# Kernel tuning notes

Measured on AMD Instinct MI355X. Metric: run time of the kernel, lower is better.

The kernel has to match this reference:

```python
import jax, jax.numpy as jnp
import numpy as np

B, L, D, V, M = 8, 64, 256, 4096, 16


def _norm(a):
    # torch .std(-1) uses ddof=1 (unbiased)
    return a / (1e-5 + jnp.std(a, axis=-1, keepdims=True, ddof=1))


def setup_inputs() -> dict:
    key = jax.random.key(0)
    ks = jax.random.split(key, 13)
    s = 0.05
    return {
        "x": jax.random.randint(ks[0], (B, L), 0, V),
        "z": jax.random.randint(ks[1], (B, L), 0, V),
        "embed_w": jax.random.normal(ks[2], (V, D), dtype=jnp.float32) * s,
        "init_w": jax.random.normal(ks[3], (D, M), dtype=jnp.float32) * s,
        "trans_w": jax.random.normal(ks[4], (D, D), dtype=jnp.float32) * s,
        "trans_b": jax.random.normal(ks[5], (D,), dtype=jnp.float32) * s,
        "core_w": jax.random.normal(ks[6], (D, D), dtype=jnp.float32) * s,
        "upd_w": jax.random.normal(ks[7], (D, D), dtype=jnp.float32) * s,
        "xks_w": jax.random.normal(ks[8], (2, D), dtype=jnp.float32) * s,
        "xkd_w": jax.random.normal(ks[9], (D, D), dtype=jnp.float32) * s,
        "xkd_b": jax.random.normal(ks[10], (D,), dtype=jnp.float32) * s,
        "emi_w": jax.random.normal(ks[11], (D, D), dtype=jnp.float32) * s,
        "emi_b": jax.random.normal(ks[12], (D,), dtype=jnp.float32) * s,
    }


def reference(x, z, embed_w, init_w, trans_w, trans_b, core_w, upd_w,
              xks_w, xkd_w, xkd_b, emi_w, emi_b):
    # loss() sets y = x * 0 (all-zero token ids)
    ze = _norm(embed_w[z])                      # (B, L, D)
    ye = _norm(embed_w[x * 0])                  # (B, L, D)
    Bq, Lq, Dq = ze.shape

    # init_state.weight.T[None, 0:1] -> column 0, broadcast to (B, L, D), then norm
    xsa0 = _norm(jnp.broadcast_to(init_w[:, 0][None, None, :], (Bq, Lq, Dq)))

    def step(xsa, _):
        xnew = (jnp.roll(xsa, 1, axis=1) @ trans_w
                + jnp.roll(xsa, -1, axis=1) @ trans_w.T
                + xsa @ core_w
                + ze @ upd_w.T
                + trans_b) / 3.0
        return xnew, None

    xsa, _ = jax.lax.scan(step, xsa0, None, length=Lq)

    # mixture head
    xkey_static = jnp.broadcast_to(xks_w[None], (Bq, 2, Dq))          # (B, 2, D)
    xkey_dynamic = ye @ xkd_w.T + xkd_b                                # (B, L, D)
    xkey = jnp.concatenate([xkey_static, xkey_dynamic], axis=1)       # (B, 2+L, D)

    emit = xsa @ emi_w.T + emi_b                                       # (B, L, D)
    cand = jnp.concatenate(
        [emit[:, :, None], ze[:, :, None],
         jnp.broadcast_to(ye[:, None], (Bq, Lq, Lq, Dq))], axis=2)     # (B, L, 2+L, D)

    sel = jax.nn.log_softmax(jnp.einsum('bld,bkd->blk', xsa, xkey), axis=-1)  # (B, L, 2+L)
    lptok_c = jax.nn.log_softmax(cand @ embed_w.T, axis=-1)            # (B, L, 2+L, V)
    lptok = jax.nn.logsumexp(sel[..., None] + lptok_c, axis=-2)        # (B, L, V)
    lptok = jnp.exp(lptok / 2.0)

    cent = jnp.take_along_axis(lptok, x[:, :, None], axis=-1)[..., 0]  # (B, L)
    return -cent.mean(-1)                                              # (B,)
```

## Files before the change

### kernel.cpp

```cpp
#include <hip/hip_runtime.h>
#include <hip/hip_bf16.h>
#include <math.h>

#define BB 8
#define LL 64
#define DD 256
#define VV 4096
#define RR 512
#define K3 768

typedef __attribute__((ext_vector_type(4))) float f32x4;
typedef __attribute__((ext_vector_type(8))) short bf16x8;
typedef __attribute__((ext_vector_type(4))) unsigned short u16x4;
typedef unsigned long long u64;

#define WS_ZE      0
#define WS_ZEU3    (WS_ZE + RR*DD)
#define WS_WCT     (WS_ZEU3 + RR*DD)
#define WS_XSA0    (WS_WCT + DD*K3)
#define WS_XSA1    (WS_XSA0 + RR*DD)
#define WS_EMIT    (WS_XSA1 + RR*DD)
#define WS_YVEC    (WS_EMIT + RR*DD)
#define WS_X0VEC   (WS_YVEC + DD)
#define WS_YK      (WS_X0VEC + DD)
#define WS_YLOG    (WS_YK + DD)
#define WS_YLSE    (WS_YLOG + VV)
#define WS_SEL     (WS_YLSE + 8)
#define WS_TOKS    WS_SEL
#define WS_HPART   WS_WCT
#define WS_TWT     WS_XSA0
#define WS_CWT     (WS_XSA0 + 65536)
#define WS_EHI     861184
#define WS_ELO     (WS_EHI + VV*DD/2)

__device__ __forceinline__ float waveSum(float v) {
#pragma unroll
  for (int o = 32; o > 0; o >>= 1) v += __shfl_xor(v, o, 64);
  return v;
}

__device__ __forceinline__ unsigned short f2bf(float f) {
  unsigned int u = __float_as_uint(f);
  unsigned int r = (u + 0x7fffu + ((u >> 16) & 1u)) >> 16;
  return (unsigned short)r;
}
__device__ __forceinline__ float bf2f(unsigned short h) {
  return __uint_as_float(((unsigned int)h) << 16);
}

union U64F2 { u64 u; float f[2]; };

__global__ __launch_bounds__(256) void k_prep1(
    const int* __restrict__ z, const float* __restrict__ embed,
    const float* __restrict__ initw, const float* __restrict__ tw,
    const float* __restrict__ cw, float* __restrict__ ws) {
  int bid = blockIdx.x, d = threadIdx.x;
  __shared__ float red[4];
  if (bid < RR + 2) {
    float a; float* dst;
    if (bid < RR) { int tok = z[bid]; a = embed[tok * DD + d]; dst = ws + WS_ZE + bid * DD; }
    else if (bid == RR) { a = embed[d]; dst = ws + WS_YVEC; }
    else { a = initw[d * 16]; dst = ws + WS_X0VEC; }
    int lane = d & 63, w = d >> 6;
    float s = waveSum(a);
    __syncthreads();
    if (lane == 0) red[w] = s;
    __syncthreads();
    float sum = red[0] + red[1] + red[2] + red[3];
    float sq = waveSum(a * a);
    __syncthreads();
    if (lane == 0) red[w] = sq;
    __syncthreads();
    float sqs = red[0] + red[1] + red[2] + red[3];
    float mean = sum * (1.0f / DD);
    float var = fmaxf((sqs - (float)DD * mean * mean) * (1.0f / (DD - 1)), 0.0f);
    dst[d] = a / (1e-5f + sqrtf(var));
  } else {
    int c = bid - (RR + 2);
    ws[WS_TWT + c * DD + d] = tw[d * DD + c];
    ws[WS_CWT + c * DD + d] = cw[d * DD + c];
  }
}

__global__ __launch_bounds__(256) void k_rowmat2(
    const float* __restrict__ in, const float* __restrict__ W,
    const float* __restrict__ bias, float* __restrict__ out, float scale) {
  int r0 = blockIdx.x * 2, d = threadIdx.x;
  __shared__ float u[2][260];
  u[0][d] = in[r0 * DD + d];
  u[1][d] = in[(r0 + 1) * DD + d];
  __syncthreads();
  float a0 = 0.f, a1 = 0.f;
  const float4* w4 = (const float4*)(W + d * DD);
  const float4* u0 = (const float4*)&u[0][0];
  const float4* u1 = (const float4*)&u[1][0];
#pragma unroll 8
  for (int k4 = 0; k4 < 64; k4++) {
    float4 w = w4[k4], x0 = u0[k4], x1 = u1[k4];
    a0 += x0.x*w.x + x0.y*w.y + x0.z*w.z + x0.w*w.w;
    a1 += x1.x*w.x + x1.y*w.y + x1.z*w.z + x1.w*w.w;
  }
  float b = bias[d];
  out[r0 * DD + d]       = (a0 + b) * scale;
  out[(r0 + 1) * DD + d] = (a1 + b) * scale;
}

__global__ __launch_bounds__(256) void k_prep3(
    const float* __restrict__ tw, const float* __restrict__ cw,
    float* __restrict__ ws) {
  int bid = blockIdx.x, c = threadIdx.x;
  __shared__ float zs[4][260];
  __shared__ float rA[DD], rB[DD], rC[DD];
  if (bid < 256) {
    int r0 = bid * 2;
    int b = r0 >> 6, l = r0 & 63;
    const float* zb = ws + WS_ZEU3 + (size_t)b * 64 * DD;
    float* zout = ws + WS_XSA1;
#pragma unroll
    for (int j = 0; j < 4; ++j) {
      int ll = (l + j - 1 + 64) & 63;
      zs[j][c] = zb[ll * DD + c];
    }
    __syncthreads();
    const float4* wA = (const float4*)(ws + WS_TWT + (size_t)c * DD);
    const float4* wB = (const float4*)(tw + (size_t)c * DD);
    const float4* wC = (const float4*)(ws + WS_CWT + (size_t)c * DD);
    const float4* zm0 = (const float4*)&zs[0][0];
    const float4* z00 = (const float4*)&zs[1][0];
    const float4* zp0 = (const float4*)&zs[2][0];
    const float4* zp1 = (const float4*)&zs[3][0];
    float a0 = 0.f, a1 = 0.f;
#pragma unroll 8
    for (int k4 = 0; k4 < 64; ++k4) {
      float4 A4 = wA[k4], B4 = wB[k4], C4 = wC[k4];
      float4 m0 = zm0[k4], z0 = z00[k4], p0 = zp0[k4], p1 = zp1[k4];
      a0 += m0.x*A4.x + m0.y*A4.y + m0.z*A4.z + m0.w*A4.w
          + p0.x*B4.x + p0.y*B4.y + p0.z*B4.z + p0.w*B4.w
          + z0.x*C4.x + z0.y*C4.y + z0.z*C4.z + z0.w*C4.w;
      a1 += z0.x*A4.x + z0.y*A4.y + z0.z*A4.z + z0.w*A4.w
          + p1.x*B4.x + p1.y*B4.y + p1.z*B4.z + p1.w*B4.w
          + p0.x*C4.x + p0.y*C4.y + p0.z*C4.z + p0.w*C4.w;
    }
    const float inv3 = 1.0f / 3.0f;
    zout[(size_t)r0 * DD + c]       = a0 * inv3 + zs[1][c];
    zout[(size_t)(r0 + 1) * DD + c] = a1 * inv3 + zs[2][c];
  } else if (bid < 512) {
    int k = bid - 256;
    const float* twT = ws + WS_TWT;
    const float inv9 = 1.0f / 9.0f;
    rA[c] = tw[k * DD + c] * inv9;
    rB[c] = twT[k * DD + c] * inv9;
    rC[c] = cw[k * DD + c] * inv9;
    __syncthreads();
    float a2 = 0.f, m1 = 0.f, m0 = 0.f, m3 = 0.f, b2 = 0.f;
#pragma unroll 4
    for (int j = 0; j < DD; ++j) {
      float Aj = tw[j * DD + c];
      float Bj = twT[j * DD + c];
      float Cj = cw[j * DD + c];
      float ra = rA[j], rb = rB[j], rc = rC[j];
      a2 += ra * Aj;
      m1 += rc * Aj + ra * Cj;
      m0 += rb * Aj + ra * Bj + rc * Cj;
      m3 += rc * Bj + rb * Cj;
      b2 += rb * Bj;
    }
    float* p0 = ws + WS_WCT;
    float* p3 = ws + WS_ZEU3;
    p0[k * DD + c]               = a2;
    p0[65536 + k * DD + c]       = m1;
    p0[2 * 65536 + k * DD + c]   = m0;
    p3[k * DD + c]               = m3;
    p3[65536 + k * DD + c]       = b2;
  } else {
    ((int*)(ws + WS_TOKS))[(bid - 512) * 256 + c] = 0;
  }
}

__global__ __launch_bounds__(256, 2) void k_scan_big(
    float* __restrict__ ws, const float* __restrict__ embed,
    const float* __restrict__ emiw, const float* __restrict__ emib) {
  const int bid = blockIdx.x;
  const int t = threadIdx.x, lane = t & 63;

  __shared__ float S[12 * 264];
  __shared__ float PAR[32 * 260];
  __shared__ float PAR2[4 * 256];
  __shared__ float ZB[256];

  if (bid >= 512) {
    int eb = bid - 512;
    if (eb < 1024) {
      unsigned short* eh = (unsigned short*)(ws + WS_EHI);
      unsigned short* el = (unsigned short*)(ws + WS_ELO);
      int i = (eb * 256 + t) * 4;
      float4 v = *(const float4*)(embed + i);
      float f[4] = {v.x, v.y, v.z, v.w};
      u16x4 h, l;
#pragma unroll
      for (int j = 0; j < 4; ++j) {
        unsigned short hb = f2bf(f[j]);
        h[j] = hb;
        l[j] = f2bf(f[j] - bf2f(hb));
      }
      *(u16x4*)(eh + i) = h;
      *(u16x4*)(el + i) = l;
    } else {
      int yb = eb - 1024;
      float* y = S;
      y[t] = ws[WS_YVEC + t];
      __syncthreads();
      int w = t >> 6;
      for (int i = 0; i < 16; i++) {
        int v = yb * 64 + i * 4 + w;
        float p = 0.f;
#pragma unroll
        for (int j = 0; j < 4; j++)
          p += y[lane + 64*j] * embed[(size_t)v * DD + lane + 64*j];
        p = waveSum(p);
        if (lane == 0) ws[WS_YLOG + v] = p;
      }
    }
    return;
  }

  const int rg = bid & 63, cg = bid >> 6;
  const int b = rg >> 3, rgl = rg & 7, l0 = rgl * 8;
  const int cl = t & 7, rs = t >> 3;
  const int c0 = cg * 32 + cl * 4;

  int* tok = (int*)(ws + WS_TOKS);

  const float* Wp[5] = {ws + WS_WCT, ws + WS_WCT + 65536, ws + WS_WCT + 2*65536,
                        ws + WS_ZEU3, ws + WS_ZEU3 + 65536};
  f32x4 wreg[40];
#pragma unroll
  for (int p = 0; p < 5; ++p)
#pragma unroll
    for (int q = 0; q < 2; ++q)
#pragma unroll
      for (int kk = 0; kk < 4; ++kk)
        wreg[p * 8 + q * 4 + kk] =
            *(const f32x4*)&Wp[p][(size_t)(rs * 8 + q * 4 + kk) * DD + c0];

  {
    int r = t >> 5, c = t & 31;
    ZB[r * 32 + c] = ws[WS_XSA1 + (size_t)(b * 64 + l0 + r) * DD + cg * 32 + c];
  }

  const int nb0 = b * 8 + ((rgl + 7) & 7);
  const int nb1 = b * 8 + rgl;
  const int nb2 = b * 8 + ((rgl + 1) & 7);
  const int myl = (lane == 0) ? nb0 : (lane == 1) ? nb1 : nb2;

  for (int st = 0; st < 32; ++st) {
    const float* xin  = ws + ((st & 1) ? WS_XSA1 : WS_XSA0);
    float*       xout = ws + ((st & 1) ? WS_XSA0 : WS_XSA1);

    if (st > 0) {
      const int tg = st << 3;
      while (true) {
        int v = __hip_atomic_load(tok + myl * 32, __ATOMIC_RELAXED,
                                  __HIP_MEMORY_SCOPE_AGENT);
        if (__all(v >= tg)) break;
        __builtin_amdgcn_s_sleep(1);
      }
    }

#pragma unroll
    for (int it = 0; it < 6; ++it) {
      int idx = it * 256 + t;
      int j = idx >> 7;
      int kk = (idx & 127) << 1;
      const u64* src = (st == 0)
          ? (const u64*)(ws + WS_X0VEC + kk)
          : (const u64*)(xin + (size_t)(b * 64 + ((l0 + j - 2 + 64) & 63)) * DD + kk);
      u64 v = __hip_atomic_load(src, __ATOMIC_RELAXED, __HIP_MEMORY_SCOPE_AGENT);
      *(u64*)(&S[j * 264 + kk]) = v;
    }
    __syncthreads();

    f32x4 acc[8];
#pragma unroll
    for (int r = 0; r < 8; ++r) acc[r] = (f32x4){0.f, 0.f, 0.f, 0.f};

#pragma unroll
    for (int p = 0; p < 5; ++p) {
#pragma unroll
      for (int r = 0; r < 8; ++r) {
        int j = r + p;
#pragma unroll
        for (int q = 0; q < 2; ++q) {
          f32x4 xv = *(const f32x4*)&S[j * 264 + rs * 8 + q * 4];
          acc[r] += xv.x * wreg[p * 8 + q * 4 + 0];
          acc[r] += xv.y * wreg[p * 8 + q * 4 + 1];
          acc[r] += xv.z * wreg[p * 8 + q * 4 + 2];
          acc[r] += xv.w * wreg[p * 8 + q * 4 + 3];
        }
      }
    }

#pragma unroll
    for (int r = 0; r < 8; ++r)
      *(f32x4*)&PAR[rs * 260 + r * 32 + cl * 4] = acc[r];
    __syncthreads();

    {
      int u = t & 63, v = t >> 6;
      f32x4 s4 = (f32x4){0.f, 0.f, 0.f, 0.f};
#pragma unroll
      for (int i = 0; i < 8; ++i)
        s4 += *(const f32x4*)&PAR[(v * 8 + i) * 260 + u * 4];
      *(f32x4*)&PAR2[v * 256 + u * 4] = s4;
    }
    __syncthreads();

    if (t < 64) {
      int r = t >> 3, c8 = t & 7;
      f32x4 s4 = (f32x4){0.f, 0.f, 0.f, 0.f};
#pragma unroll
      for (int v = 0; v < 4; ++v)
        s4 += *(const f32x4*)&PAR2[v * 256 + t * 4];
      f32x4 zb = *(const f32x4*)&ZB[r * 32 + c8 * 4];
      s4 += zb;
      size_t off = (size_t)(b * 64 + l0 + r) * DD + cg * 32 + c8 * 4;
      U64F2 lo, hi;
      lo.f[0] = s4.x; lo.f[1] = s4.y;
      hi.f[0] = s4.z; hi.f[1] = s4.w;
      __hip_atomic_store((u64*)(xout + off),     lo.u, __ATOMIC_RELAXED, __HIP_MEMORY_SCOPE_AGENT);
      __hip_atomic_store((u64*)(xout + off + 2), hi.u, __ATOMIC_RELAXED, __HIP_MEMORY_SCOPE_AGENT);
    }

    __syncthreads();
    if (t == 0)
      __hip_atomic_fetch_add(tok + nb1 * 32, 1, __ATOMIC_RELAXED,
                             __HIP_MEMORY_SCOPE_AGENT);
  }

  if (t == 0) {
    while (__hip_atomic_load(tok + nb1 * 32, __ATOMIC_RELAXED,
                             __HIP_MEMORY_SCOPE_AGENT) < 256)
      __builtin_amdgcn_s_sleep(1);
  }
  __syncthreads();
#pragma unroll
  for (int it = 0; it < 4; ++it) {
    int idx = it * 256 + t;
    int j = idx >> 7;
    int kk = (idx & 127) << 1;
    u64 v = __hip_atomic_load(
        (const u64*)(ws + WS_XSA0 + (size_t)(b * 64 + l0 + j) * DD + kk),
        __ATOMIC_RELAXED, __HIP_MEMORY_SCOPE_AGENT);
    *(u64*)(&S[j * 264 + kk]) = v;
  }
  __syncthreads();
  {
    int r = t >> 5, c = cg * 32 + (t & 31);
    const float4* wv = (const float4*)(emiw + (size_t)c * DD);
    const float4* xv = (const float4*)&S[r * 264];
    float a = 0.f;
#pragma unroll 8
    for (int k4 = 0; k4 < 64; ++k4) {
      float4 w = wv[k4], x = xv[k4];
      a += x.x*w.x + x.y*w.y + x.z*w.z + x.w*w.w;
    }
    ws[WS_EMIT + (size_t)(b * 64 + l0 + r) * DD + c] = a + emib[c];
  }
}

__global__ __launch_bounds__(256) void k_head_mfma(
    const float* __restrict__ uemit, const float* __restrict__ uze,
    const unsigned short* __restrict__ eh, const unsigned short* __restrict__ el,
    float* __restrict__ hpart) {
  int row0 = blockIdx.x * 32;
  int v0 = blockIdx.y * 128;
  int t = threadIdx.x, lane = t & 63, w = t >> 6;
  int wr = w >> 1, wc = w & 1;
  __shared__ unsigned short UH[32 * 264];
  __shared__ unsigned short UL[32 * 264];
  const float* src = (row0 < RR) ? (uemit + (size_t)row0 * DD)
                                 : (uze + (size_t)(row0 - RR) * DD);
#pragma unroll
  for (int it = 0; it < 4; ++it) {
    int r = it * 8 + (t >> 5);
    int c8 = (t & 31) * 8;
    float4 a = *(const float4*)(src + (size_t)r * DD + c8);
    float4 b2 = *(const float4*)(src + (size_t)r * DD + c8 + 4);
    float fa[8] = {a.x, a.y, a.z, a.w, b2.x, b2.y, b2.z, b2.w};
    u16x4 h0, l0v, h1, l1;
#pragma unroll
    for (int j = 0; j < 4; ++j) {
      unsigned short hb = f2bf(fa[j]);
      h0[j] = hb; l0v[j] = f2bf(fa[j] - bf2f(hb));
      unsigned short hb1 = f2bf(fa[4 + j]);
      h1[j] = hb1; l1[j] = f2bf(fa[4 + j] - bf2f(hb1));
    }
    *(u16x4*)(&UH[r * 264 + c8])     = h0;
    *(u16x4*)(&UH[r * 264 + c8 + 4]) = h1;
    *(u16x4*)(&UL[r * 264 + c8])     = l0v;
    *(u16x4*)(&UL[r * 264 + c8 + 4]) = l1;
  }
  __syncthreads();

  f32x4 acc[4];
#pragma unroll
  for (int q = 0; q < 4; ++q) acc[q] = (f32x4){0.f, 0.f, 0.f, 0.f};

  int arow = wr * 16 + (lane & 15);
  int kof = 8 * (lane >> 4);
  const unsigned short* Ah = &UH[arow * 264 + kof];
  const unsigned short* Al = &UL[arow * 264 + kof];
  int vbase = v0 + wc * 64 + (lane & 15);

#pragma unroll
  for (int p = 0; p < 3; ++p) {
    const unsigned short* Ab = (p == 2) ? Al : Ah;
    const unsigned short* Ebl = ((p == 1) ? el : eh) + (size_t)vbase * DD + kof;
#pragma unroll
    for (int ks = 0; ks < 8; ++ks) {
      int k0 = ks * 32;
      bf16x8 a = *(const bf16x8*)(Ab + k0);
#pragma unroll
      for (int vt = 0; vt < 4; ++vt) {
        bf16x8 bfr = *(const bf16x8*)(Ebl + vt * 16 * DD + k0);
        acc[vt] = __builtin_amdgcn_mfma_f32_16x16x32_bf16(a, bfr, acc[vt], 0, 0, 0);
      }
    }
  }

  int chunk = blockIdx.y * 2 + wc;
#pragma unroll
  for (int i = 0; i < 4; ++i) {
    float mm = -1e30f;
#pragma unroll
    for (int vt = 0; vt < 4; ++vt) mm = fmaxf(mm, acc[vt][i]);
#pragma unroll
    for (int o = 1; o < 16; o <<= 1) mm = fmaxf(mm, __shfl_xor(mm, o, 64));
    float ss = 0.f;
#pragma unroll
    for (int vt = 0; vt < 4; ++vt) ss += __expf(acc[vt][i] - mm);
#pragma unroll
    for (int o = 1; o < 16; o <<= 1) ss += __shfl_xor(ss, o, 64);
    if ((lane & 15) == 0) {
      int row = row0 + wr * 16 + (lane >> 4) * 4 + i;
      hpart[(row * 64 + chunk) * 2]     = mm;
      hpart[(row * 64 + chunk) * 2 + 1] = ss;
    }
  }
}

__global__ __launch_bounds__(256) void k_finish(
    const int* __restrict__ x, const float* __restrict__ embed,
    const float* __restrict__ xks, const float* __restrict__ xkdw,
    const float* __restrict__ xkdb, float* __restrict__ ws,
    float* __restrict__ out) {
  int b = blockIdx.x, t = threadIdx.x, lane = t & 63, w = t >> 6;
  __shared__ float YK[DD];
  __shared__ float rm[4], rv[4];
  __shared__ float ylse_s;
  __shared__ float sel0[64], sel1[64], sel2[64], tg0[64], tg1[64];
  __shared__ float ls0s[64], ls1s[64];

  {
    float acc = xkdb[t];
    const float4* yv4 = (const float4*)(ws + WS_YVEC);
    const float4* w4 = (const float4*)(xkdw + (size_t)t * DD);
    float a = 0.f;
#pragma unroll 8
    for (int k4 = 0; k4 < 64; ++k4) {
      float4 yv = yv4[k4], wv = w4[k4];
      a += yv.x*wv.x + yv.y*wv.y + yv.z*wv.z + yv.w*wv.w;
    }
    YK[t] = acc + a;
  }
  {
    float m = -1e30f, s = 0.f;
    for (int v = t; v < VV; v += 256) {
      float lg = ws[WS_YLOG + v];
      float mn = fmaxf(m, lg);
      s = s * __expf(m - mn) + __expf(lg - mn);
      m = mn;
    }
#pragma unroll
    for (int o = 32; o > 0; o >>= 1) {
      float mo = __shfl_xor(m, o, 64), so = __shfl_xor(s, o, 64);
      float mn = fmaxf(m, mo);
      s = s * __expf(m - mn) + so * __expf(mo - mn);
      m = mn;
    }
    if (lane == 0) { rm[w] = m; rv[w] = s; }
  }
  __syncthreads();
  if (t == 0) {
    float M = fmaxf(fmaxf(rm[0], rm[1]), fmaxf(rm[2], rm[3]));
    float S = rv[0]*__expf(rm[0]-M) + rv[1]*__expf(rm[1]-M) +
              rv[2]*__expf(rm[2]-M) + rv[3]*__expf(rm[3]-M);
    ylse_s = M + logf(S);
  }

  const float* hp = ws + WS_HPART;
  for (int i = 0; i < 16; ++i) {
    int l = w * 16 + i, r = b * 64 + l;
    float4 xs = *(const float4*)&ws[WS_XSA0 + (size_t)r * DD + lane * 4];
    float4 k0 = *(const float4*)&xks[lane * 4];
    float4 k1 = *(const float4*)&xks[DD + lane * 4];
    float4 yk4 = *(const float4*)&YK[lane * 4];
    float s0 = waveSum(xs.x*k0.x + xs.y*k0.y + xs.z*k0.z + xs.w*k0.w);
    float s1 = waveSum(xs.x*k1.x + xs.y*k1.y + xs.z*k1.z + xs.w*k1.w);
    float s2 = waveSum(xs.x*yk4.x + xs.y*yk4.y + xs.z*yk4.z + xs.w*yk4.w);
    int xv = x[r];
    float4 e4 = *(const float4*)&embed[(size_t)xv * DD + lane * 4];
    float4 em = *(const float4*)&ws[WS_EMIT + (size_t)r * DD + lane * 4];
    float4 zr = *(const float4*)&ws[WS_ZE + (size_t)r * DD + lane * 4];
    float t0 = waveSum(em.x*e4.x + em.y*e4.y + em.z*e4.z + em.w*e4.w);
    float t1 = waveSum(zr.x*e4.x + zr.y*e4.y + zr.z*e4.z + zr.w*e4.w);
    float m0 = hp[((size_t)r * 64 + lane) * 2];
    float q0 = hp[((size_t)r * 64 + lane) * 2 + 1];
    float m1 = hp[((size_t)(RR + r) * 64 + lane) * 2];
    float q1 = hp[((size_t)(RR + r) * 64 + lane) * 2 + 1];
#pragma unroll
    for (int o = 32; o > 0; o >>= 1) {
      float mo = __shfl_xor(m0, o, 64), so = __shfl_xor(q0, o, 64);
      float mn = fmaxf(m0, mo);
      q0 = q0 * __expf(m0 - mn) + so * __expf(mo - mn);
      m0 = mn;
      mo = __shfl_xor(m1, o, 64); so = __shfl_xor(q1, o, 64);
      mn = fmaxf(m1, mo);
      q1 = q1 * __expf(m1 - mn) + so * __expf(mo - mn);
      m1 = mn;
    }
    if (lane == 0) {
      sel0[l] = s0; sel1[l] = s1; sel2[l] = s2;
      tg0[l] = t0; tg1[l] = t1;
      ls0s[l] = m0 + logf(q0);
      ls1s[l] = m1 + logf(q1);
    }
  }
  __syncthreads();
  if (w == 0) {
    int l = lane, r = b * 64 + l;
    float s0 = sel0[l], s1 = sel1[l], s2 = sel2[l];
    float mx = fmaxf(s0, fmaxf(s1, s2));
    float den = expf(s0 - mx) + expf(s1 - mx) + 64.f * expf(s2 - mx);
    float lsel = mx + logf(den);
    int xv = x[r];
    float P0 = expf(s0 - lsel + tg0[l] - ls0s[l]);
    float P1 = expf(s1 - lsel + tg1[l] - ls1s[l]);
    float Py = expf(s2 - lsel + ws[WS_YLOG + xv] - ylse_s);
    float cent = sqrtf(P0 + P1 + 64.f * Py);
    float sum = waveSum(cent);
    if (lane == 0) out[b] = -(sum * (1.0f / 64.f));
  }
}

extern "C" void kernel_launch(void* const* d_in, const int* in_sizes, int n_in,
                              void* d_out, int out_size, void* d_ws, size_t ws_size,
                              hipStream_t stream) {
  (void)in_sizes; (void)n_in; (void)out_size; (void)ws_size;
  const int*   x     = (const int*)d_in[0];
  const int*   z     = (const int*)d_in[1];
  const float* embed = (const float*)d_in[2];
  const float* initw = (const float*)d_in[3];
  const float* tw    = (const float*)d_in[4];
  const float* tb    = (const float*)d_in[5];
  const float* cw    = (const float*)d_in[6];
  const float* uw    = (const float*)d_in[7];
  const float* xks   = (const float*)d_in[8];
  const float* xkdw  = (const float*)d_in[9];
  const float* xkdb  = (const float*)d_in[10];
  const float* emiw  = (const float*)d_in[11];
  const float* emib  = (const float*)d_in[12];
  float* ws  = (float*)d_ws;
  float* out = (float*)d_out;

  hipLaunchKernelGGL(k_prep1, dim3(RR + 2 + 256), dim3(256), 0, stream,
                     z, embed, initw, tw, cw, ws);
  hipLaunchKernelGGL(k_rowmat2, dim3(256), dim3(256), 0, stream,
                     ws + WS_ZE, uw, tb, ws + WS_ZEU3, 1.0f / 3.0f);
  hipLaunchKernelGGL(k_prep3, dim3(520), dim3(256), 0, stream, tw, cw, ws);
  hipLaunchKernelGGL(k_scan_big, dim3(1600), dim3(256), 0, stream,
                     ws, embed, emiw, emib);
  hipLaunchKernelGGL(k_head_mfma, dim3(32, 32), dim3(256), 0, stream,
                     ws + WS_EMIT, ws + WS_ZE,
                     (const unsigned short*)(ws + WS_EHI),
                     (const unsigned short*)(ws + WS_ELO),
                     ws + WS_HPART);
  hipLaunchKernelGGL(k_finish, dim3(8), dim3(256), 0, stream,
                     x, embed, xks, xkdw, xkdb, ws, out);
}
```

Measured before the change: 353.4 us.

## Overlap ze-row head tiles with the scan and move embed prep earlier

Moves the bf16 hi/lo split of the embedding and the y-logit computation out of the scan kernel into the prep kernel, with a new tiny kernel that normalizes the y and x0 vectors first. When the workspace is large enough, the half of the head GEMM that depends only on ze rows runs as extra blocks inside the scan kernel, with partial results written to a separate buffer, so it overlaps the latency-bound scan. The separate head kernel then covers only the emit rows. This adds a launch, relies on workspace size to choose the path, and could cost scan occupancy through the shared memory union.

```diff
diff --git a/kernel.cpp b/kernel.cpp
--- a/kernel.cpp
+++ b/kernel.cpp
@@ -27,11 +27,12 @@
 #define WS_YLSE    (WS_YLOG + VV)
 #define WS_SEL     (WS_YLSE + 8)
 #define WS_TOKS    WS_SEL
-#define WS_HPART   WS_WCT
 #define WS_TWT     WS_XSA0
 #define WS_CWT     (WS_XSA0 + 65536)
 #define WS_EHI     861184
 #define WS_ELO     (WS_EHI + VV*DD/2)
+#define WS_HPHI    (WS_ELO + VV*DD/2)
+#define WS_BIG_FLOATS (WS_HPHI + 1024*64*2)
 
 __device__ __forceinline__ float waveSum(float v) {
 #pragma unroll
@@ -49,6 +50,86 @@
 }
 
 union U64F2 { u64 u; float f[2]; };
+
+__device__ __forceinline__ void head_tile(
+    int row0, int vy, const float* __restrict__ uemit,
+    const float* __restrict__ uze,
+    const unsigned short* __restrict__ eh, const unsigned short* __restrict__ el,
+    float* __restrict__ hpart, float* shbuf, int t) {
+  unsigned short* UH = (unsigned short*)shbuf;
+  unsigned short* UL = UH + 32 * 264;
+  int lane = t & 63, w = t >> 6;
+  int wr = w >> 1, wc = w & 1;
+  const float* src = (row0 < RR) ? (uemit + (size_t)row0 * DD)
+                                 : (uze + (size_t)(row0 - RR) * DD);
+#pragma unroll
+  for (int it = 0; it < 4; ++it) {
+    int r = it * 8 + (t >> 5);
+    int c8 = (t & 31) * 8;
+    float4 a = *(const float4*)(src + (size_t)r * DD + c8);
+    float4 b2 = *(const float4*)(src + (size_t)r * DD + c8 + 4);
+    float fa[8] = {a.x, a.y, a.z, a.w, b2.x, b2.y, b2.z, b2.w};
+    u16x4 h0, l0v, h1, l1;
+#pragma unroll
+    for (int j = 0; j < 4; ++j) {
+      unsigned short hb = f2bf(fa[j]);
+      h0[j] = hb; l0v[j] = f2bf(fa[j] - bf2f(hb));
+      unsigned short hb1 = f2bf(fa[4 + j]);
+      h1[j] = hb1; l1[j] = f2bf(fa[4 + j] - bf2f(hb1));
+    }
+    *(u16x4*)(&UH[r * 264 + c8])     = h0;
+    *(u16x4*)(&UH[r * 264 + c8 + 4]) = h1;
+    *(u16x4*)(&UL[r * 264 + c8])     = l0v;
+    *(u16x4*)(&UL[r * 264 + c8 + 4]) = l1;
+  }
+  __syncthreads();
+
+  f32x4 acc[4];
+#pragma unroll
+  for (int q = 0; q < 4; ++q) acc[q] = (f32x4){0.f, 0.f, 0.f, 0.f};
+
+  int arow = wr * 16 + (lane & 15);
+  int kof = 8 * (lane >> 4);
+  const unsigned short* Ah = &UH[arow * 264 + kof];
+  const unsigned short* Al = &UL[arow * 264 + kof];
+  int vbase = vy * 128 + wc * 64 + (lane & 15);
+
+#pragma unroll
+  for (int p = 0; p < 3; ++p) {
+    const unsigned short* Ab = (p == 2) ? Al : Ah;
+    const unsigned short* Ebl = ((p == 1) ? el : eh) + (size_t)vbase * DD + kof;
+#pragma unroll
+    for (int ks = 0; ks < 8; ++ks) {
+      int k0 = ks * 32;
+      bf16x8 a = *(const bf16x8*)(Ab + k0);
+#pragma unroll
+      for (int vt = 0; vt < 4; ++vt) {
+        bf16x8 bfr = *(const bf16x8*)(Ebl + vt * 16 * DD + k0);
+        acc[vt] = __builtin_amdgcn_mfma_f32_16x16x32_bf16(a, bfr, acc[vt], 0, 0, 0);
+      }
+    }
+  }
+
+  int chunk = vy * 2 + wc;
+#pragma unroll
+  for (int i = 0; i < 4; ++i) {
+    float mm = -1e30f;
+#pragma unroll
+    for (int vt = 0; vt < 4; ++vt) mm = fmaxf(mm, acc[vt][i]);
+#pragma unroll
+    for (int o = 1; o < 16; o <<= 1) mm = fmaxf(mm, __shfl_xor(mm, o, 64));
+    float ss = 0.f;
+#pragma unroll
+    for (int vt = 0; vt < 4; ++vt) ss += __expf(acc[vt][i] - mm);
+#pragma unroll
+    for (int o = 1; o < 16; o <<= 1) ss += __shfl_xor(ss, o, 64);
+    if ((lane & 15) == 0) {
+      int row = row0 + wr * 16 + (lane >> 4) * 4 + i;
+      hpart[((size_t)row * 64 + chunk) * 2]     = mm;
+      hpart[((size_t)row * 64 + chunk) * 2 + 1] = ss;
+    }
+  }
+}
 
 __global__ __launch_bounds__(256) void k_prep1(
     const int* __restrict__ z, const float* __restrict__ embed,
@@ -56,6 +137,7 @@
     const float* __restrict__ cw, float* __restrict__ ws) {
   int bid = blockIdx.x, d = threadIdx.x;
   __shared__ float red[4];
+  __shared__ float y[DD];
   if (bid < RR + 2) {
     float a; float* dst;
     if (bid < RR) { int tok = z[bid]; a = embed[tok * DD + d]; dst = ws + WS_ZE + bid * DD; }
@@ -75,11 +157,64 @@
     float mean = sum * (1.0f / DD);
     float var = fmaxf((sqs - (float)DD * mean * mean) * (1.0f / (DD - 1)), 0.0f);
     dst[d] = a / (1e-5f + sqrtf(var));
-  } else {
+  } else if (bid < RR + 2 + 256) {
     int c = bid - (RR + 2);
     ws[WS_TWT + c * DD + d] = tw[d * DD + c];
     ws[WS_CWT + c * DD + d] = cw[d * DD + c];
-  }
+  } else if (bid < RR + 2 + 256 + 1024) {
+    int eb = bid - (RR + 2 + 256);
+    unsigned short* eh = (unsigned short*)(ws + WS_EHI);
+    unsigned short* el = (unsigned short*)(ws + WS_ELO);
+    int i = (eb * 256 + d) * 4;
+    float4 v = *(const float4*)(embed + i);
+    float f[4] = {v.x, v.y, v.z, v.w};
+    u16x4 h, l;
+#pragma unroll
+    for (int j = 0; j < 4; ++j) {
+      unsigned short hb = f2bf(f[j]);
+      h[j] = hb;
+      l[j] = f2bf(f[j] - bf2f(hb));
+    }
+    *(u16x4*)(eh + i) = h;
+    *(u16x4*)(el + i) = l;
+  } else {
+    int yb = bid - (RR + 2 + 256 + 1024);
+    y[d] = ws[WS_YVEC + d];
+    __syncthreads();
+    int w = d >> 6, lane = d & 63;
+    for (int i = 0; i < 16; i++) {
+      int v = yb * 64 + i * 4 + w;
+      float p = 0.f;
+#pragma unroll
+      for (int j = 0; j < 4; j++)
+        p += y[lane + 64*j] * embed[(size_t)v * DD + lane + 64*j];
+      p = waveSum(p);
+      if (lane == 0) ws[WS_YLOG + v] = p;
+    }
+  }
+}
+
+__global__ __launch_bounds__(256) void k_prep0(
+    const float* __restrict__ embed, const float* __restrict__ initw,
+    float* __restrict__ ws) {
+  int r = blockIdx.x, d = threadIdx.x;
+  __shared__ float red[4];
+  float a = (r == 0) ? embed[d] : initw[d * 16];
+  float* dst = ws + ((r == 0) ? WS_YVEC : WS_X0VEC);
+  int lane = d & 63, w = d >> 6;
+  float s = waveSum(a);
+  __syncthreads();
+  if (lane == 0) red[w] = s;
+  __syncthreads();
+  float sum = red[0] + red[1] + red[2] + red[3];
+  float sq = waveSum(a * a);
+  __syncthreads();
+  if (lane == 0) red[w] = sq;
+  __syncthreads();
+  float sqs = red[0] + red[1] + red[2] + red[3];
+  float mean = sum * (1.0f / DD);
+  float var = fmaxf((sqs - (float)DD * mean * mean) * (1.0f / (DD - 1)), 0.0f);
+  dst[d] = a / (1e-5f + sqrtf(var));
 }
 
 __global__ __launch_bounds__(256) void k_rowmat2(
@@ -178,51 +313,26 @@
 }
 
 __global__ __launch_bounds__(256, 2) void k_scan_big(
-    float* __restrict__ ws, const float* __restrict__ embed,
-    const float* __restrict__ emiw, const float* __restrict__ emib) {
+    float* __restrict__ ws, const float* __restrict__ emiw,
+    const float* __restrict__ emib, const unsigned short* __restrict__ eh,
+    const unsigned short* __restrict__ el, float* __restrict__ hpart) {
   const int bid = blockIdx.x;
   const int t = threadIdx.x, lane = t & 63;
 
-  __shared__ float S[12 * 264];
-  __shared__ float PAR[32 * 260];
-  __shared__ float PAR2[4 * 256];
-  __shared__ float ZB[256];
+  __shared__ float SH[12800];
 
   if (bid >= 512) {
     int eb = bid - 512;
-    if (eb < 1024) {
-      unsigned short* eh = (unsigned short*)(ws + WS_EHI);
-      unsigned short* el = (unsigned short*)(ws + WS_ELO);
-      int i = (eb * 256 + t) * 4;
-      float4 v = *(const float4*)(embed + i);
-      float f[4] = {v.x, v.y, v.z, v.w};
-      u16x4 h, l;
-#pragma unroll
-      for (int j = 0; j < 4; ++j) {
-        unsigned short hb = f2bf(f[j]);
-        h[j] = hb;
-        l[j] = f2bf(f[j] - bf2f(hb));
-      }
-      *(u16x4*)(eh + i) = h;
-      *(u16x4*)(el + i) = l;
-    } else {
-      int yb = eb - 1024;
-      float* y = S;
-      y[t] = ws[WS_YVEC + t];
-      __syncthreads();
-      int w = t >> 6;
-      for (int i = 0; i < 16; i++) {
-        int v = yb * 64 + i * 4 + w;
-        float p = 0.f;
-#pragma unroll
-        for (int j = 0; j < 4; j++)
-          p += y[lane + 64*j] * embed[(size_t)v * DD + lane + 64*j];
-        p = waveSum(p);
-        if (lane == 0) ws[WS_YLOG + v] = p;
-      }
-    }
+    int row0 = RR + (eb & 15) * 32;
+    int vy = eb >> 4;
+    head_tile(row0, vy, ws + WS_EMIT, ws + WS_ZE, eh, el, hpart, SH, t);
     return;
   }
+
+  float* S    = SH;
+  float* PAR  = SH + 3168;
+  float* PAR2 = SH + 11488;
+  float* ZB   = SH + 12512;
 
   const int rg = bid & 63, cg = bid >> 6;
   const int b = rg >> 3, rgl = rg & 7, l0 = rgl * 8;
@@ -372,88 +482,16 @@
     const float* __restrict__ uemit, const float* __restrict__ uze,
     const unsigned short* __restrict__ eh, const unsigned short* __restrict__ el,
     float* __restrict__ hpart) {
-  int row0 = blockIdx.x * 32;
-  int v0 = blockIdx.y * 128;
-  int t = threadIdx.x, lane = t & 63, w = t >> 6;
-  int wr = w >> 1, wc = w & 1;
-  __shared__ unsigned short UH[32 * 264];
-  __shared__ unsigned short UL[32 * 264];
-  const float* src = (row0 < RR) ? (uemit + (size_t)row0 * DD)
-                                 : (uze + (size_t)(row0 - RR) * DD);
-#pragma unroll
-  for (int it = 0; it < 4; ++it) {
-    int r = it * 8 + (t >> 5);
-    int c8 = (t & 31) * 8;
-    float4 a = *(const float4*)(src + (size_t)r * DD + c8);
-    float4 b2 = *(const float4*)(src + (size_t)r * DD + c8 + 4);
-    float fa[8] = {a.x, a.y, a.z, a.w, b2.x, b2.y, b2.z, b2.w};
-    u16x4 h0, l0v, h1, l1;
-#pragma unroll
-    for (int j = 0; j < 4; ++j) {
-      unsigned short hb = f2bf(fa[j]);
-      h0[j] = hb; l0v[j] = f2bf(fa[j] - bf2f(hb));
-      unsigned short hb1 = f2bf(fa[4 + j]);
-      h1[j] = hb1; l1[j] = f2bf(fa[4 + j] - bf2f(hb1));
-    }
-    *(u16x4*)(&UH[r * 264 + c8])     = h0;
-    *(u16x4*)(&UH[r * 264 + c8 + 4]) = h1;
-    *(u16x4*)(&UL[r * 264 + c8])     = l0v;
-    *(u16x4*)(&UL[r * 264 + c8 + 4]) = l1;
-  }
-  __syncthreads();
-
-  f32x4 acc[4];
-#pragma unroll
-  for (int q = 0; q < 4; ++q) acc[q] = (f32x4){0.f, 0.f, 0.f, 0.f};
-
-  int arow = wr * 16 + (lane & 15);
-  int kof = 8 * (lane >> 4);
-  const unsigned short* Ah = &UH[arow * 264 + kof];
-  const unsigned short* Al = &UL[arow * 264 + kof];
-  int vbase = v0 + wc * 64 + (lane & 15);
-
-#pragma unroll
-  for (int p = 0; p < 3; ++p) {
-    const unsigned short* Ab = (p == 2) ? Al : Ah;
-    const unsigned short* Ebl = ((p == 1) ? el : eh) + (size_t)vbase * DD + kof;
-#pragma unroll
-    for (int ks = 0; ks < 8; ++ks) {
-      int k0 = ks * 32;
-      bf16x8 a = *(const bf16x8*)(Ab + k0);
-#pragma unroll
-      for (int vt = 0; vt < 4; ++vt) {
-        bf16x8 bfr = *(const bf16x8*)(Ebl + vt * 16 * DD + k0);
-        acc[vt] = __builtin_amdgcn_mfma_f32_16x16x32_bf16(a, bfr, acc[vt], 0, 0, 0);
-      }
-    }
-  }
-
-  int chunk = blockIdx.y * 2 + wc;
-#pragma unroll
-  for (int i = 0; i < 4; ++i) {
-    float mm = -1e30f;
-#pragma unroll
-    for (int vt = 0; vt < 4; ++vt) mm = fmaxf(mm, acc[vt][i]);
-#pragma unroll
-    for (int o = 1; o < 16; o <<= 1) mm = fmaxf(mm, __shfl_xor(mm, o, 64));
-    float ss = 0.f;
-#pragma unroll
-    for (int vt = 0; vt < 4; ++vt) ss += __expf(acc[vt][i] - mm);
-#pragma unroll
-    for (int o = 1; o < 16; o <<= 1) ss += __shfl_xor(ss, o, 64);
-    if ((lane & 15) == 0) {
-      int row = row0 + wr * 16 + (lane >> 4) * 4 + i;
-      hpart[(row * 64 + chunk) * 2]     = mm;
-      hpart[(row * 64 + chunk) * 2 + 1] = ss;
-    }
-  }
+  __shared__ float SH[8448];
+  head_tile(blockIdx.x * 32, blockIdx.y, uemit, uze, eh, el, hpart, SH,
+            threadIdx.x);
 }
 
 __global__ __launch_bounds__(256) void k_finish(
     const int* __restrict__ x, const float* __restrict__ embed,
     const float* __restrict__ xks, const float* __restrict__ xkdw,
     const float* __restrict__ xkdb, float* __restrict__ ws,
-    float* __restrict__ out) {
+    const float* __restrict__ hp, float* __restrict__ out) {
   int b = blockIdx.x, t = threadIdx.x, lane = t & 63, w = t >> 6;
   __shared__ float YK[DD];
   __shared__ float rm[4], rv[4];
@@ -498,7 +536,6 @@
     ylse_s = M + logf(S);
   }
 
-  const float* hp = ws + WS_HPART;
   for (int i = 0; i < 16; ++i) {
     int l = w * 16 + i, r = b * 64 + l;
     float4 xs = *(const float4*)&ws[WS_XSA0 + (size_t)r * DD + lane * 4];
@@ -556,7 +593,7 @@
 extern "C" void kernel_launch(void* const* d_in, const int* in_sizes, int n_in,
                               void* d_out, int out_size, void* d_ws, size_t ws_size,
                               hipStream_t stream) {
-  (void)in_sizes; (void)n_in; (void)out_size; (void)ws_size;
+  (void)in_sizes; (void)n_in; (void)out_size;
   const int*   x     = (const int*)d_in[0];
   const int*   z     = (const int*)d_in[1];
   const float* embed = (const float*)d_in[2];
@@ -573,18 +610,21 @@
   float* ws  = (float*)d_ws;
   float* out = (float*)d_out;
 
-  hipLaunchKernelGGL(k_prep1, dim3(RR + 2 + 256), dim3(256), 0, stream,
-                     z, embed, initw, tw, cw, ws);
+  const bool big = ws_size >= (size_t)WS_BIG_FLOATS * sizeof(float);
+  float* hpart = ws + (big ? WS_HPHI : WS_WCT);
+  const unsigned short* ehg = (const unsigned short*)(ws + WS_EHI);
+  const unsigned short* elg = (const unsigned short*)(ws + WS_ELO);
+
+  hipLaunchKernelGGL(k_prep0, dim3(2), dim3(256), 0, stream, embed, initw, ws);
+  hipLaunchKernelGGL(k_prep1, dim3(RR + 2 + 256 + 1024 + 64), dim3(256), 0,
+                     stream, z, embed, initw, tw, cw, ws);
   hipLaunchKernelGGL(k_rowmat2, dim3(256), dim3(256), 0, stream,
                      ws + WS_ZE, uw, tb, ws + WS_ZEU3, 1.0f / 3.0f);
   hipLaunchKernelGGL(k_prep3, dim3(520), dim3(256), 0, stream, tw, cw, ws);
-  hipLaunchKernelGGL(k_scan_big, dim3(1600), dim3(256), 0, stream,
-                     ws, embed, emiw, emib);
-  hipLaunchKernelGGL(k_head_mfma, dim3(32, 32), dim3(256), 0, stream,
-                     ws + WS_EMIT, ws + WS_ZE,
-                     (const unsigned short*)(ws + WS_EHI),
-                     (const unsigned short*)(ws + WS_ELO),
-                     ws + WS_HPART);
+  hipLaunchKernelGGL(k_scan_big, dim3(big ? 1024 : 512), dim3(256), 0, stream,
+                     ws, emiw, emib, ehg, elg, hpart);
+  hipLaunchKernelGGL(k_head_mfma, dim3(big ? 16 : 32, 32), dim3(256), 0, stream,
+                     ws + WS_EMIT, ws + WS_ZE, ehg, elg, hpart);
   hipLaunchKernelGGL(k_finish, dim3(8), dim3(256), 0, stream,
-                     x, embed, xks, xkdw, xkdb, ws, out);
-}
+                     x, embed, xks, xkdw, xkdb, ws, hpart, out);
+}
```

Measured after the change: 352.0 us. No clear change (-0.4%).
